# Performance work log

Hardware: AMD Instinct MI355X
Metric: run time of the kernel (lower is better)

## Reference

```python
import jax, jax.numpy as jnp
import numpy as np

H = 8  # num_heads

def layernorm(x, g, b, eps=1e-5):
    mu = jnp.mean(x, axis=-1, keepdims=True)
    var = jnp.var(x, axis=-1, keepdims=True)
    return (x - mu) * jax.lax.rsqrt(var + eps) * g + b

def mha(x, w_in, b_in, w_out, b_out, bias=None):
    # x: [B_, S, D]; w_in: [3D, D] packed q,k,v (PyTorch MHA layout)
    B_, S, D = x.shape
    hd = D // H
    qkv = x @ w_in.T + b_in                      # [B_, S, 3D]
    q, k, v = jnp.split(qkv, 3, axis=-1)
    def heads(t):
        return t.reshape(B_, S, H, hd).transpose(0, 2, 1, 3)  # [B_, H, S, hd]
    q, k, v = heads(q), heads(k), heads(v)
    scores = jnp.einsum('bhqd,bhkd->bhqk', q, k) / jnp.sqrt(jnp.float32(hd))
    if bias is not None:
        scores = scores + bias[None, None]        # broadcast [S,S] bias
    attn = jax.nn.softmax(scores, axis=-1)
    out = jnp.einsum('bhqk,bhkd->bhqd', attn, v)  # [B_, H, S, hd]
    out = out.transpose(0, 2, 1, 3).reshape(B_, S, D)
    return out @ w_out.T + b_out

def setup_inputs() -> dict:
    key = jax.random.key(0)
    ks = jax.random.split(key, 8)
    B, T, N, D, F = 32, 12, 325, 128, 512
    s = 0.05
    return {
        'x': jax.random.normal(ks[0], (B, T, N, D), jnp.float32),
        't_w_in': jax.random.normal(ks[1], (3 * D, D), jnp.float32) * s,
        't_b_in': jnp.zeros((3 * D,), jnp.float32),
        't_w_out': jax.random.normal(ks[2], (D, D), jnp.float32) * s,
        't_b_out': jnp.zeros((D,), jnp.float32),
        's_w_in': jax.random.normal(ks[3], (3 * D, D), jnp.float32) * s,
        's_b_in': jnp.zeros((3 * D,), jnp.float32),
        's_w_out': jax.random.normal(ks[4], (D, D), jnp.float32) * s,
        's_b_out': jnp.zeros((D,), jnp.float32),
        'g_bias': jax.random.normal(ks[5], (N, N), jnp.float32) * 0.5,
        'norm_t_g': jnp.ones((D,), jnp.float32),
        'norm_t_b': jnp.zeros((D,), jnp.float32),
        'norm_s_g': jnp.ones((D,), jnp.float32),
        'norm_s_b': jnp.zeros((D,), jnp.float32),
        'ff_w1': jax.random.normal(ks[6], (F, D), jnp.float32) * s,
        'ff_b1': jnp.zeros((F,), jnp.float32),
        'ff_w2': jax.random.normal(ks[7], (D, F), jnp.float32) * s,
        'ff_b2': jnp.zeros((D,), jnp.float32),
        'norm_ff_g': jnp.ones((D,), jnp.float32),
        'norm_ff_b': jnp.zeros((D,), jnp.float32),
    }

def reference(x, t_w_in, t_b_in, t_w_out, t_b_out, s_w_in, s_b_in, s_w_out, s_b_out,
              g_bias, norm_t_g, norm_t_b, norm_s_g, norm_s_b,
              ff_w1, ff_b1, ff_w2, ff_b2, norm_ff_g, norm_ff_b):
    B, T, N, D = x.shape
    # Temporal attention: each sensor attends over time
    xt = x.transpose(0, 2, 1, 3).reshape(B * N, T, D)
    xt = mha(xt, t_w_in, t_b_in, t_w_out, t_b_out)
    x = layernorm(x + xt.reshape(B, N, T, D).transpose(0, 2, 1, 3), norm_t_g, norm_t_b)
    # Spatial attention with graph bias: each timestep attends over sensors
    xs = x.reshape(B * T, N, D)
    xs = mha(xs, s_w_in, s_b_in, s_w_out, s_b_out, bias=g_bias)
    x = layernorm(x + xs.reshape(B, T, N, D), norm_s_g, norm_s_b)
    # FFN
    h = jax.nn.gelu(x @ ff_w1.T + ff_b1) @ ff_w2.T + ff_b2
    x = layernorm(x + h, norm_ff_g, norm_ff_b)
    return x
```

## Files before the change

kernel.cpp:

```cpp
#include <hip/hip_runtime.h>
#include <cstdint>
#include <cstddef>


#define B_ 32
#define T_ 12
#define N_ 325
#define D_ 128
#define H_ 8
#define F_ 512
#define NT 124800
#define BCH 8
#define CHK (BCH * T_ * N_)
#define NCHUNK 4
#define GT ((CHK + 63) / 64)
#define NKT 11
#define NQT 21

#define O_XBF 0UL
#define O_Y1B 31948800UL
#define O_QKV 63897600UL
#define O_ABUF 87859200UL
#define O_WB 95846400UL
#define O_PB 96370688UL

typedef __attribute__((ext_vector_type(8))) short bf16x8;
typedef __attribute__((ext_vector_type(4))) float f32x4;

__device__ inline float b2f(unsigned short b) {
  unsigned int u = ((unsigned int)b) << 16;
  return __builtin_bit_cast(float, u);
}
__device__ inline unsigned short f2b(float f) {
  unsigned int u = __builtin_bit_cast(unsigned int, f);
  unsigned int r = (u + 0x7FFFu + ((u >> 16) & 1u)) >> 16;
  return (unsigned short)r;
}
__device__ inline f32x4 mfma16(bf16x8 a, bf16x8 b, f32x4 c) {
  return __builtin_amdgcn_mfma_f32_16x16x32_bf16(a, b, c, 0, 0, 0);
}
__device__ inline float gelu_t(float x) {
  float x3 = x * x * x;
  return 0.5f * x * (1.0f + tanhf(0.7978845608f * (x + 0.044715f * x3)));
}

__global__ void k_convert(const void* __restrict__ src, float* __restrict__ dF,
                          unsigned short* __restrict__ dB, long n,
                          const unsigned short* __restrict__ probe) {
  long i = (long)blockIdx.x * blockDim.x + threadIdx.x;
  if (i >= n) return;
  bool isbf = probe[0] != 0;
  float v = isbf ? b2f(((const unsigned short*)src)[i]) : ((const float*)src)[i];
  if (dF) dF[i] = v;
  if (dB) dB[i] = f2b(v);
}

__global__ void k_conv_params(
    const void* s1, const void* s2, const void* s3, const void* s4,
    const void* s5, const void* s6, const void* s7, const void* s8,
    const void* s9, const void* s10, const void* s11, const void* s12,
    const void* s13, const void* s14, const void* s15, const void* s16,
    const void* s17, const void* s18, const void* s19, char* ws,
    const unsigned short* __restrict__ probe) {
  long i = (long)blockIdx.x * blockDim.x + threadIdx.x;
  bool isbf = probe[0] != 0;
  long o = 0;
#define LOADV(src, j) \
  (isbf ? b2f(((const unsigned short*)(src))[j]) : ((const float*)(src))[j])
#define SEGB(src, dstoff, n)                                        \
  if (i < o + (n)) {                                                \
    long j = i - o;                                                 \
    ((unsigned short*)(ws + (dstoff)))[j] = f2b(LOADV(src, j));     \
    return;                                                         \
  }                                                                 \
  o += (n);
#define SEGF(src, dstoff, n)                              \
  if (i < o + (n)) {                                      \
    long j = i - o;                                       \
    ((float*)(ws + (dstoff)))[j] = LOADV(src, j);         \
    return;                                               \
  }                                                       \
  o += (n);
  SEGB(s1, O_WB + 0, 49152)
  SEGF(s2, O_PB + 0, 384)
  SEGB(s3, O_WB + 98304, 16384)
  SEGF(s4, O_PB + 1536, 128)
  SEGB(s5, O_WB + 131072, 49152)
  SEGF(s6, O_PB + 2048, 384)
  SEGB(s7, O_WB + 229376, 16384)
  SEGF(s8, O_PB + 3584, 128)
  SEGF(s9, O_PB + 9728, 105625)
  SEGF(s10, O_PB + 6656, 128)
  SEGF(s11, O_PB + 7168, 128)
  SEGF(s12, O_PB + 7680, 128)
  SEGF(s13, O_PB + 8192, 128)
  SEGB(s14, O_WB + 262144, 65536)
  SEGF(s15, O_PB + 4096, 512)
  SEGB(s16, O_WB + 393216, 65536)
  SEGF(s17, O_PB + 6144, 128)
  SEGF(s18, O_PB + 8704, 128)
  SEGF(s19, O_PB + 9216, 128)
#undef SEGB
#undef SEGF
#undef LOADV
}
#define CONVP_TOTAL 370201L

template <int ROWS, int KTOT>
__device__ inline void stage_tile(short (*dst)[ROWS][32],
                                  const unsigned short* __restrict__ src,
                                  int row0, int k0, int tid, int Mrows) {
  constexpr int CH = ROWS * 16;
#pragma unroll
  for (int it = 0; it < CH / 256; ++it) {
    int cb = tid + it * 256;
    int row = cb >> 4;
    int kc = cb & 15;
    int gr = row0 + row;
    gr = gr < Mrows ? gr : Mrows - 1;
    uint4 v = *(const uint4*)(src + (size_t)gr * KTOT + (size_t)k0 + kc * 8);
    *(uint4*)(&dst[kc >> 2][row][(kc & 3) * 8]) = v;
  }
}

template <int KTOT, bool GELU>
__global__ __launch_bounds__(256) void k_gemm_store(
    const unsigned short* __restrict__ Ab, const unsigned short* __restrict__ Wb,
    const float* __restrict__ bias, unsigned short* __restrict__ outB, int Ntot,
    int Mrows, int Nrows) {
  __shared__ __align__(16) union USm {
    struct { short A[4][64][32]; short B[4][64][32]; } s;
    float C[64][68];
  } sm;
  const int tid = threadIdx.x;
  const int m0 = blockIdx.x * 64;
  const int n0 = blockIdx.y * 64;
  const int lane = tid & 63, wave = tid >> 6;
  const int wm = wave >> 1, wn = wave & 1;
  const int ml = lane & 15, quad = lane >> 4;
  f32x4 acc[2][2] = {};
#pragma unroll
  for (int c = 0; c < KTOT / 128; ++c) {
    if (c) __syncthreads();
    stage_tile<64, KTOT>(sm.s.A, Ab, m0, c * 128, tid, Mrows);
    stage_tile<64, KTOT>(sm.s.B, Wb, n0, c * 128, tid, Nrows);
    __syncthreads();
#pragma unroll
    for (int kc = 0; kc < 4; ++kc) {
      bf16x8 a0 = *(const bf16x8*)&sm.s.A[kc][wm * 32 + ml][quad * 8];
      bf16x8 a1 = *(const bf16x8*)&sm.s.A[kc][wm * 32 + 16 + ml][quad * 8];
      bf16x8 b0 = *(const bf16x8*)&sm.s.B[kc][wn * 32 + ml][quad * 8];
      bf16x8 b1 = *(const bf16x8*)&sm.s.B[kc][wn * 32 + 16 + ml][quad * 8];
      acc[0][0] = mfma16(a0, b0, acc[0][0]);
      acc[0][1] = mfma16(a0, b1, acc[0][1]);
      acc[1][0] = mfma16(a1, b0, acc[1][0]);
      acc[1][1] = mfma16(a1, b1, acc[1][1]);
    }
  }
  __syncthreads();
#pragma unroll
  for (int mi = 0; mi < 2; ++mi)
#pragma unroll
    for (int ni = 0; ni < 2; ++ni)
#pragma unroll
      for (int r = 0; r < 4; ++r)
        sm.C[wm * 32 + mi * 16 + quad * 4 + r][wn * 32 + ni * 16 + ml] =
            acc[mi][ni][r];
  __syncthreads();
  const int trow = tid >> 4;
  const int tcol = (tid & 15) * 4;
  const float4 bv = *(const float4*)&bias[n0 + tcol];
#pragma unroll
  for (int it = 0; it < 4; ++it) {
    int row = it * 16 + trow;
    int gm = m0 + row;
    float4 cv = *(const float4*)&sm.C[row][tcol];
    float v0 = cv.x + bv.x, v1 = cv.y + bv.y, v2 = cv.z + bv.z,
          v3 = cv.w + bv.w;
    if (GELU) {
      v0 = gelu_t(v0); v1 = gelu_t(v1); v2 = gelu_t(v2); v3 = gelu_t(v3);
    }
    if (gm < Mrows) {
      ushort4 ov;
      ov.x = f2b(v0); ov.y = f2b(v1); ov.z = f2b(v2); ov.w = f2b(v3);
      *(ushort4*)&outB[(size_t)gm * Ntot + n0 + tcol] = ov;
    }
  }
}

template <int KTOT, bool FINAL>
__global__ __launch_bounds__(256) void k_gemm_ln(
    const unsigned short* __restrict__ Ab, const unsigned short* __restrict__ Wb,
    const float* __restrict__ bias, const unsigned short* __restrict__ resid,
    const float* __restrict__ gamma, const float* __restrict__ beta,
    unsigned short* __restrict__ outB, void* __restrict__ dOut, size_t row0g,
    const unsigned short* __restrict__ probe, int Mrows) {
  __shared__ __align__(16) union USm {
    struct { short A[4][64][32]; short B[4][128][32]; } s;
    float C[64][132];
  } sm;
  const int tid = threadIdx.x;
  const int m0 = blockIdx.x * 64;
  const int lane = tid & 63, wave = tid >> 6;
  const int wm = wave >> 1, wn = wave & 1;
  const int ml = lane & 15, quad = lane >> 4;
  f32x4 acc[2][4] = {};
#pragma unroll
  for (int c = 0; c < KTOT / 128; ++c) {
    if (c) __syncthreads();
    stage_tile<64, KTOT>(sm.s.A, Ab, m0, c * 128, tid, Mrows);
    stage_tile<128, KTOT>(sm.s.B, Wb, 0, c * 128, tid, 128);
    __syncthreads();
#pragma unroll
    for (int kc = 0; kc < 4; ++kc) {
      bf16x8 a[2], b[4];
#pragma unroll
      for (int mi = 0; mi < 2; ++mi)
        a[mi] = *(const bf16x8*)&sm.s.A[kc][wm * 32 + mi * 16 + ml][quad * 8];
#pragma unroll
      for (int ni = 0; ni < 4; ++ni)
        b[ni] = *(const bf16x8*)&sm.s.B[kc][wn * 64 + ni * 16 + ml][quad * 8];
#pragma unroll
      for (int mi = 0; mi < 2; ++mi)
#pragma unroll
        for (int ni = 0; ni < 4; ++ni)
          acc[mi][ni] = mfma16(a[mi], b[ni], acc[mi][ni]);
    }
  }
  __syncthreads();
#pragma unroll
  for (int mi = 0; mi < 2; ++mi)
#pragma unroll
    for (int ni = 0; ni < 4; ++ni)
#pragma unroll
      for (int r = 0; r < 4; ++r)
        sm.C[wm * 32 + mi * 16 + quad * 4 + r][wn * 64 + ni * 16 + ml] =
            acc[mi][ni][r];
  __syncthreads();
  const int c0 = lane * 2;
  const float bia0 = bias[c0], bia1 = bias[c0 + 1];
  const float ga0 = gamma[c0], ga1 = gamma[c0 + 1];
  const float be0 = beta[c0], be1 = beta[c0 + 1];
  const bool isbf = FINAL ? (probe[0] != 0) : true;
#pragma unroll
  for (int rr = 0; rr < 16; ++rr) {
    int row = wave * 16 + rr;
    int gm = m0 + row;
    bool valid = gm < Mrows;
    float2 cc = *(const float2*)&sm.C[row][c0];
    float r0 = 0.f, r1 = 0.f;
    if (valid) {
      ushort2 rv = *(const ushort2*)&resid[(size_t)gm * 128 + c0];
      r0 = b2f(rv.x);
      r1 = b2f(rv.y);
    }
    float v0 = cc.x + bia0 + r0, v1 = cc.y + bia1 + r1;
    float s = v0 + v1, q = v0 * v0 + v1 * v1;
#pragma unroll
    for (int off = 1; off < 64; off <<= 1) {
      s += __shfl_xor(s, off);
      q += __shfl_xor(q, off);
    }
    float mean = s * (1.f / 128.f);
    float var = q * (1.f / 128.f) - mean * mean;
    float rs = rsqrtf(var + 1e-5f);
    float y0 = (v0 - mean) * rs * ga0 + be0;
    float y1 = (v1 - mean) * rs * ga1 + be1;
    if (valid) {
      if (FINAL) {
        if (isbf) {
          ushort2 ov; ov.x = f2b(y0); ov.y = f2b(y1);
          *(ushort2*)((unsigned short*)dOut + (row0g + gm) * 128 + c0) = ov;
        } else {
          float2 ov; ov.x = y0; ov.y = y1;
          *(float2*)((float*)dOut + (row0g + gm) * 128 + c0) = ov;
        }
      } else {
        ushort2 ov; ov.x = f2b(y0); ov.y = f2b(y1);
        *(ushort2*)&outB[(size_t)gm * 128 + c0] = ov;
      }
    }
  }
}

__global__ __launch_bounds__(128) void k_attn_t(
    const unsigned short* __restrict__ qkv, unsigned short* __restrict__ A) {
  __shared__ float ls[12][384];
  const int tid = threadIdx.x;
  const int bx = blockIdx.x;
  const int b = bx / N_, n = bx % N_;
  for (int i = tid; i < 12 * 384; i += 128) {
    int t = i / 384, c = i % 384;
    size_t tok = (size_t)(b * T_ + t) * N_ + n;
    ls[t][c] = b2f(qkv[tok * 384 + c]);
  }
  __syncthreads();
  if (tid < 96) {
    int h = tid / 12, q = tid % 12;
    const float* qv = &ls[q][h * 16];
    float s[12];
    float m = -1e30f;
#pragma unroll
    for (int t = 0; t < 12; ++t) {
      float d = 0.f;
#pragma unroll
      for (int dd = 0; dd < 16; ++dd) d += qv[dd] * ls[t][128 + h * 16 + dd];
      s[t] = d * 0.25f;
      m = fmaxf(m, s[t]);
    }
    float l = 0.f;
#pragma unroll
    for (int t = 0; t < 12; ++t) {
      s[t] = __expf(s[t] - m);
      l += s[t];
    }
    float inv = 1.0f / l;
    size_t otok = (size_t)(b * T_ + q) * N_ + n;
#pragma unroll
    for (int dd = 0; dd < 16; ++dd) {
      float o = 0.f;
#pragma unroll
      for (int t = 0; t < 12; ++t) o += s[t] * ls[t][256 + h * 16 + dd];
      A[otok * 128 + h * 16 + dd] = f2b(o * inv);
    }
  }
}

__global__ __launch_bounds__(256) void k_attn_s(
    const unsigned short* __restrict__ qkv, const float* __restrict__ gbias,
    unsigned short* __restrict__ A) {
  __shared__ short Ks[352 * 24];
  __shared__ short Vt[16 * 360];
  __shared__ short Ps[4][16 * 40];
  __shared__ uint4 zq;
  const int tid = threadIdx.x;
  const int bt = blockIdx.x, h = blockIdx.y;
  const size_t base = (size_t)bt * N_;
  for (int i = tid; i < 352 * 2; i += 256) {
    int s = i >> 1, half = i & 1;
    if (s < N_) {
      size_t rb = (base + s) * 384 + h * 16 + half * 8;
      uint4 kv = *(const uint4*)(qkv + rb + 128);
      *(uint4*)&Ks[s * 24 + half * 8] = kv;
      uint4 vv = *(const uint4*)(qkv + rb + 256);
      const unsigned short* vs = (const unsigned short*)&vv;
#pragma unroll
      for (int e = 0; e < 8; ++e) Vt[(half * 8 + e) * 360 + s] = vs[e];
    } else {
      *(uint4*)&Ks[s * 24 + half * 8] = uint4{0, 0, 0, 0};
#pragma unroll
      for (int e = 0; e < 8; ++e) Vt[(half * 8 + e) * 360 + s] = 0;
    }
  }
  if (tid == 0) zq = uint4{0, 0, 0, 0};
  __syncthreads();
  const int lane = tid & 63, wave = tid >> 6;
  const int ml = lane & 15, quad = lane >> 4;
  const f32x4 fz = {0.f, 0.f, 0.f, 0.f};
  short* myP = Ps[wave];
  for (int qt = wave; qt < NQT; qt += 4) {
    bf16x8 qfrag = {0, 0, 0, 0, 0, 0, 0, 0};
    int qrow = qt * 16 + ml;
    qrow = qrow < N_ ? qrow : N_ - 1;
    if (quad < 2)
      qfrag = *(const bf16x8*)(qkv + (base + qrow) * 384 + h * 16 + quad * 8);
    f32x4 O = fz;
    float lsum[4] = {0.f, 0.f, 0.f, 0.f};
    for (int kt = 0; kt < NKT; ++kt) {
      const short* kp0 =
          (quad < 2) ? &Ks[(kt * 32 + ml) * 24 + quad * 8] : (const short*)&zq;
      const short* kp1 = (quad < 2) ? &Ks[(kt * 32 + 16 + ml) * 24 + quad * 8]
                                    : (const short*)&zq;
      bf16x8 kf0 = *(const bf16x8*)kp0;
      bf16x8 kf1 = *(const bf16x8*)kp1;
      f32x4 S1 = mfma16(qfrag, kf0, fz);
      f32x4 S2 = mfma16(qfrag, kf1, fz);
      int s0 = kt * 32 + ml, s1g = s0 + 16;
      int sa0 = s0 < N_ ? s0 : N_ - 1;
      int sa1 = s1g < N_ ? s1g : N_ - 1;
      float p1[4], p2[4];
#pragma unroll
      for (int r = 0; r < 4; ++r) {
        int qg = qt * 16 + quad * 4 + r;
        qg = qg < N_ ? qg : N_ - 1;
        const float* brow = gbias + (size_t)qg * N_;
        p1[r] = __expf(S1[r] * 0.25f + brow[sa0]);
        p2[r] = __expf(S2[r] * 0.25f + brow[sa1]);
      }
      if (kt == NKT - 1) {
#pragma unroll
        for (int r = 0; r < 4; ++r) {
          if (s0 >= N_) p1[r] = 0.f;
          if (s1g >= N_) p2[r] = 0.f;
        }
      }
#pragma unroll
      for (int r = 0; r < 4; ++r) {
        lsum[r] += p1[r] + p2[r];
        myP[(quad * 4 + r) * 40 + ml] = (short)f2b(p1[r]);
        myP[(quad * 4 + r) * 40 + 16 + ml] = (short)f2b(p2[r]);
      }
      __builtin_amdgcn_sched_barrier(0);
      bf16x8 pf = *(const bf16x8*)&myP[ml * 40 + quad * 8];
      bf16x8 vf = *(const bf16x8*)&Vt[ml * 360 + kt * 32 + quad * 8];
      O = mfma16(pf, vf, O);
      __builtin_amdgcn_sched_barrier(0);
    }
#pragma unroll
    for (int r = 0; r < 4; ++r) {
      float v = lsum[r];
      v += __shfl_xor(v, 1);
      v += __shfl_xor(v, 2);
      v += __shfl_xor(v, 4);
      v += __shfl_xor(v, 8);
      int qg = qt * 16 + quad * 4 + r;
      if (qg < N_)
        A[(base + qg) * 128 + h * 16 + ml] = f2b(O[r] * (1.f / v));
    }
  }
}

extern "C" void kernel_launch(void* const* d_in, const int* in_sizes, int n_in,
                              void* d_out, int out_size, void* d_ws,
                              size_t ws_size, hipStream_t stream) {
  char* ws = (char*)d_ws;
  const unsigned short* probe = (const unsigned short*)d_in[10];

  unsigned short* xbf = (unsigned short*)(ws + O_XBF);
  unsigned short* y1b = (unsigned short*)(ws + O_Y1B);
  unsigned short* qkvc = (unsigned short*)(ws + O_QKV);
  unsigned short* Abufc = (unsigned short*)(ws + O_ABUF);
  unsigned short* hbuf = qkvc;
  unsigned short* y2b = xbf;
  char* wb = ws + O_WB;
  unsigned short* wt_in = (unsigned short*)(wb + 0);
  unsigned short* wt_out = (unsigned short*)(wb + 98304);
  unsigned short* wsp_in = (unsigned short*)(wb + 131072);
  unsigned short* wsp_out = (unsigned short*)(wb + 229376);
  unsigned short* wff1 = (unsigned short*)(wb + 262144);
  unsigned short* wff2 = (unsigned short*)(wb + 393216);
  char* pb = ws + O_PB;
  float* p_t_b_in = (float*)(pb + 0);
  float* p_t_b_out = (float*)(pb + 1536);
  float* p_s_b_in = (float*)(pb + 2048);
  float* p_s_b_out = (float*)(pb + 3584);
  float* p_ff_b1 = (float*)(pb + 4096);
  float* p_ff_b2 = (float*)(pb + 6144);
  float* p_ntg = (float*)(pb + 6656);
  float* p_ntb = (float*)(pb + 7168);
  float* p_nsg = (float*)(pb + 7680);
  float* p_nsb = (float*)(pb + 8192);
  float* p_nfg = (float*)(pb + 8704);
  float* p_nfb = (float*)(pb + 9216);
  float* p_gbias = (float*)(pb + 9728);

  {
    long n = (long)NT * 128;
    k_convert<<<dim3((unsigned)((n + 255) / 256)), dim3(256), 0, stream>>>(
        d_in[0], nullptr, xbf, n, probe);
    k_conv_params<<<dim3((unsigned)((CONVP_TOTAL + 255) / 256)), dim3(256), 0,
                    stream>>>(d_in[1], d_in[2], d_in[3], d_in[4], d_in[5],
                              d_in[6], d_in[7], d_in[8], d_in[9], d_in[10],
                              d_in[11], d_in[12], d_in[13], d_in[14], d_in[15],
                              d_in[16], d_in[17], d_in[18], d_in[19], ws,
                              probe);
  }

  dim3 blk(256);
  for (int c = 0; c < NCHUNK; ++c) {
    size_t tok0 = (size_t)c * CHK;
    k_gemm_store<128, false><<<dim3(GT, 6), blk, 0, stream>>>(
        xbf + tok0 * 128, wt_in, p_t_b_in, qkvc, 384, CHK, 384);
    k_attn_t<<<dim3(BCH * N_), dim3(128), 0, stream>>>(qkvc, Abufc);
    k_gemm_ln<128, false><<<dim3(GT), blk, 0, stream>>>(
        Abufc, wt_out, p_t_b_out, xbf + tok0 * 128, p_ntg, p_ntb,
        y1b + tok0 * 128, nullptr, 0, probe, CHK);
  }
  for (int c = 0; c < NCHUNK; ++c) {
    size_t tok0 = (size_t)c * CHK;
    k_gemm_store<128, false><<<dim3(GT, 6), blk, 0, stream>>>(
        y1b + tok0 * 128, wsp_in, p_s_b_in, qkvc, 384, CHK, 384);
    k_attn_s<<<dim3(BCH * T_, H_), blk, 0, stream>>>(qkvc, p_gbias, Abufc);
    k_gemm_ln<128, false><<<dim3(GT), blk, 0, stream>>>(
        Abufc, wsp_out, p_s_b_out, y1b + tok0 * 128, p_nsg, p_nsb,
        y2b + tok0 * 128, nullptr, 0, probe, CHK);
  }
  for (int c = 0; c < NCHUNK; ++c) {
    size_t tok0 = (size_t)c * CHK;
    k_gemm_store<128, true><<<dim3(GT, 8), blk, 0, stream>>>(
        y2b + tok0 * 128, wff1, p_ff_b1, hbuf, 512, CHK, 512);
    k_gemm_ln<512, true><<<dim3(GT), blk, 0, stream>>>(
        hbuf, wff2, p_ff_b2, y2b + tok0 * 128, p_nfg, p_nfb, nullptr, d_out,
        tok0, probe, CHK);
  }
}
```

Before: 841.4 us.

## Transpose spatial attention MFMA to keep probabilities in registers, pad bias rows

```diff
diff --git a/kernel.cpp b/kernel.cpp
--- a/kernel.cpp
+++ b/kernel.cpp
@@ -16,6 +16,7 @@
 #define GT ((CHK + 63) / 64)
 #define NKT 11
 #define NQT 21
+#define GBS 328
 
 #define O_XBF 0UL
 #define O_Y1B 31948800UL
@@ -25,6 +26,7 @@
 #define O_PB 96370688UL
 
 typedef __attribute__((ext_vector_type(8))) short bf16x8;
+typedef __attribute__((ext_vector_type(4))) short bf16x4;
 typedef __attribute__((ext_vector_type(4))) float f32x4;
 
 __device__ inline float b2f(unsigned short b) {
@@ -39,6 +41,19 @@
 __device__ inline f32x4 mfma16(bf16x8 a, bf16x8 b, f32x4 c) {
   return __builtin_amdgcn_mfma_f32_16x16x32_bf16(a, b, c, 0, 0, 0);
 }
+#if __has_builtin(__builtin_amdgcn_mfma_f32_16x16x16bf16_1k)
+__device__ inline f32x4 mfma16k16(bf16x4 a, bf16x4 b, f32x4 c) {
+  return __builtin_amdgcn_mfma_f32_16x16x16bf16_1k(a, b, c, 0, 0, 0);
+}
+#else
+__device__ inline f32x4 mfma16k16(bf16x4 a, bf16x4 b, f32x4 c) {
+  f32x4 d;
+  asm volatile("v_mfma_f32_16x16x16_bf16 %0, %1, %2, %3\ns_nop 7\ns_nop 7"
+               : "=v"(d)
+               : "v"(a), "v"(b), "v"(c));
+  return d;
+}
+#endif
 __device__ inline float gelu_t(float x) {
   float x3 = x * x * x;
   return 0.5f * x * (1.0f + tanhf(0.7978845608f * (x + 0.044715f * x3)));
@@ -89,7 +104,14 @@
   SEGF(s6, O_PB + 2048, 384)
   SEGB(s7, O_WB + 229376, 16384)
   SEGF(s8, O_PB + 3584, 128)
-  SEGF(s9, O_PB + 9728, 105625)
+  if (i < o + 105625) {
+    long j = i - o;
+    int q = (int)(j / 325);
+    int s = (int)(j - (long)q * 325);
+    ((float*)(ws + O_PB + 9728))[(size_t)q * GBS + s] = LOADV(s9, j);
+    return;
+  }
+  o += 105625;
   SEGF(s10, O_PB + 6656, 128)
   SEGF(s11, O_PB + 7168, 128)
   SEGF(s12, O_PB + 7680, 128)
@@ -289,10 +311,15 @@
   const int tid = threadIdx.x;
   const int bx = blockIdx.x;
   const int b = bx / N_, n = bx % N_;
-  for (int i = tid; i < 12 * 384; i += 128) {
-    int t = i / 384, c = i % 384;
+  for (int i = tid; i < 576; i += 128) {
+    int t = i / 48, c = (i % 48) * 8;
     size_t tok = (size_t)(b * T_ + t) * N_ + n;
-    ls[t][c] = b2f(qkv[tok * 384 + c]);
+    uint4 v = *(const uint4*)(qkv + tok * 384 + c);
+    const unsigned short* pv = (const unsigned short*)&v;
+    float4 f0 = {b2f(pv[0]), b2f(pv[1]), b2f(pv[2]), b2f(pv[3])};
+    float4 f1 = {b2f(pv[4]), b2f(pv[5]), b2f(pv[6]), b2f(pv[7])};
+    *(float4*)&ls[t][c] = f0;
+    *(float4*)&ls[t][c + 4] = f1;
   }
   __syncthreads();
   if (tid < 96) {
@@ -315,23 +342,30 @@
       l += s[t];
     }
     float inv = 1.0f / l;
+    float o[16];
+#pragma unroll
+    for (int dd = 0; dd < 16; ++dd) {
+      float acc = 0.f;
+#pragma unroll
+      for (int t = 0; t < 12; ++t) acc += s[t] * ls[t][256 + h * 16 + dd];
+      o[dd] = acc * inv;
+    }
     size_t otok = (size_t)(b * T_ + q) * N_ + n;
 #pragma unroll
-    for (int dd = 0; dd < 16; ++dd) {
-      float o = 0.f;
-#pragma unroll
-      for (int t = 0; t < 12; ++t) o += s[t] * ls[t][256 + h * 16 + dd];
-      A[otok * 128 + h * 16 + dd] = f2b(o * inv);
+    for (int g = 0; g < 4; ++g) {
+      ushort4 ov;
+      ov.x = f2b(o[g * 4 + 0]); ov.y = f2b(o[g * 4 + 1]);
+      ov.z = f2b(o[g * 4 + 2]); ov.w = f2b(o[g * 4 + 3]);
+      *(ushort4*)&A[otok * 128 + h * 16 + g * 4] = ov;
     }
   }
 }
 
 __global__ __launch_bounds__(256) void k_attn_s(
-    const unsigned short* __restrict__ qkv, const float* __restrict__ gbias,
+    const unsigned short* __restrict__ qkv, const float* __restrict__ gbp,
     unsigned short* __restrict__ A) {
   __shared__ short Ks[352 * 24];
-  __shared__ short Vt[16 * 360];
-  __shared__ short Ps[4][16 * 40];
+  __shared__ short Vt[16 * 364];
   __shared__ uint4 zq;
   const int tid = threadIdx.x;
   const int bt = blockIdx.x, h = blockIdx.y;
@@ -345,11 +379,11 @@
       uint4 vv = *(const uint4*)(qkv + rb + 256);
       const unsigned short* vs = (const unsigned short*)&vv;
 #pragma unroll
-      for (int e = 0; e < 8; ++e) Vt[(half * 8 + e) * 360 + s] = vs[e];
+      for (int e = 0; e < 8; ++e) Vt[(half * 8 + e) * 364 + s] = vs[e];
     } else {
       *(uint4*)&Ks[s * 24 + half * 8] = uint4{0, 0, 0, 0};
 #pragma unroll
-      for (int e = 0; e < 8; ++e) Vt[(half * 8 + e) * 360 + s] = 0;
+      for (int e = 0; e < 8; ++e) Vt[(half * 8 + e) * 364 + s] = 0;
     }
   }
   if (tid == 0) zq = uint4{0, 0, 0, 0};
@@ -357,65 +391,62 @@
   const int lane = tid & 63, wave = tid >> 6;
   const int ml = lane & 15, quad = lane >> 4;
   const f32x4 fz = {0.f, 0.f, 0.f, 0.f};
-  short* myP = Ps[wave];
   for (int qt = wave; qt < NQT; qt += 4) {
+    int q = qt * 16 + ml;
+    int qc = q < N_ ? q : N_ - 1;
     bf16x8 qfrag = {0, 0, 0, 0, 0, 0, 0, 0};
-    int qrow = qt * 16 + ml;
-    qrow = qrow < N_ ? qrow : N_ - 1;
     if (quad < 2)
-      qfrag = *(const bf16x8*)(qkv + (base + qrow) * 384 + h * 16 + quad * 8);
+      qfrag = *(const bf16x8*)(qkv + (base + qc) * 384 + h * 16 + quad * 8);
+    const float* gb = gbp + (size_t)qc * GBS;
     f32x4 O = fz;
-    float lsum[4] = {0.f, 0.f, 0.f, 0.f};
+    float lsum = 0.f;
     for (int kt = 0; kt < NKT; ++kt) {
+      const int sb = kt * 32;
       const short* kp0 =
-          (quad < 2) ? &Ks[(kt * 32 + ml) * 24 + quad * 8] : (const short*)&zq;
-      const short* kp1 = (quad < 2) ? &Ks[(kt * 32 + 16 + ml) * 24 + quad * 8]
-                                    : (const short*)&zq;
+          (quad < 2) ? &Ks[(sb + ml) * 24 + quad * 8] : (const short*)&zq;
+      const short* kp1 =
+          (quad < 2) ? &Ks[(sb + 16 + ml) * 24 + quad * 8] : (const short*)&zq;
       bf16x8 kf0 = *(const bf16x8*)kp0;
       bf16x8 kf1 = *(const bf16x8*)kp1;
-      f32x4 S1 = mfma16(qfrag, kf0, fz);
-      f32x4 S2 = mfma16(qfrag, kf1, fz);
-      int s0 = kt * 32 + ml, s1g = s0 + 16;
-      int sa0 = s0 < N_ ? s0 : N_ - 1;
-      int sa1 = s1g < N_ ? s1g : N_ - 1;
-      float p1[4], p2[4];
-#pragma unroll
-      for (int r = 0; r < 4; ++r) {
-        int qg = qt * 16 + quad * 4 + r;
-        qg = qg < N_ ? qg : N_ - 1;
-        const float* brow = gbias + (size_t)qg * N_;
-        p1[r] = __expf(S1[r] * 0.25f + brow[sa0]);
-        p2[r] = __expf(S2[r] * 0.25f + brow[sa1]);
-      }
+      f32x4 S0 = mfma16(kf0, qfrag, fz);
+      f32x4 S1 = mfma16(kf1, qfrag, fz);
+      float4 g0 = *(const float4*)&gb[sb + quad * 4];
+      const int sb1 = (sb + 16 <= 292) ? sb + 16 : 292;
+      float4 g1 = *(const float4*)&gb[sb1 + quad * 4];
+      float p0[4], p1[4];
+      p0[0] = __expf(S0[0] * 0.25f + g0.x);
+      p0[1] = __expf(S0[1] * 0.25f + g0.y);
+      p0[2] = __expf(S0[2] * 0.25f + g0.z);
+      p0[3] = __expf(S0[3] * 0.25f + g0.w);
+      p1[0] = __expf(S1[0] * 0.25f + g1.x);
+      p1[1] = __expf(S1[1] * 0.25f + g1.y);
+      p1[2] = __expf(S1[2] * 0.25f + g1.z);
+      p1[3] = __expf(S1[3] * 0.25f + g1.w);
       if (kt == NKT - 1) {
 #pragma unroll
         for (int r = 0; r < 4; ++r) {
-          if (s0 >= N_) p1[r] = 0.f;
-          if (s1g >= N_) p2[r] = 0.f;
+          if (sb + quad * 4 + r >= N_) p0[r] = 0.f;
+          p1[r] = 0.f;
         }
       }
-#pragma unroll
-      for (int r = 0; r < 4; ++r) {
-        lsum[r] += p1[r] + p2[r];
-        myP[(quad * 4 + r) * 40 + ml] = (short)f2b(p1[r]);
-        myP[(quad * 4 + r) * 40 + 16 + ml] = (short)f2b(p2[r]);
-      }
-      __builtin_amdgcn_sched_barrier(0);
-      bf16x8 pf = *(const bf16x8*)&myP[ml * 40 + quad * 8];
-      bf16x8 vf = *(const bf16x8*)&Vt[ml * 360 + kt * 32 + quad * 8];
-      O = mfma16(pf, vf, O);
-      __builtin_amdgcn_sched_barrier(0);
-    }
+      lsum += p0[0] + p0[1] + p0[2] + p0[3] + p1[0] + p1[1] + p1[2] + p1[3];
+      bf16x4 a0 = {(short)f2b(p0[0]), (short)f2b(p0[1]), (short)f2b(p0[2]),
+                   (short)f2b(p0[3])};
+      bf16x4 a1 = {(short)f2b(p1[0]), (short)f2b(p1[1]), (short)f2b(p1[2]),
+                   (short)f2b(p1[3])};
+      bf16x4 v0 = *(const bf16x4*)&Vt[ml * 364 + sb + quad * 4];
+      bf16x4 v1 = *(const bf16x4*)&Vt[ml * 364 + sb + 16 + quad * 4];
+      O = mfma16k16(a0, v0, O);
+      O = mfma16k16(a1, v1, O);
+    }
+    lsum += __shfl_xor(lsum, 16);
+    lsum += __shfl_xor(lsum, 32);
 #pragma unroll
     for (int r = 0; r < 4; ++r) {
-      float v = lsum[r];
-      v += __shfl_xor(v, 1);
-      v += __shfl_xor(v, 2);
-      v += __shfl_xor(v, 4);
-      v += __shfl_xor(v, 8);
       int qg = qt * 16 + quad * 4 + r;
+      float sr = __shfl(lsum, quad * 4 + r);
       if (qg < N_)
-        A[(base + qg) * 128 + h * 16 + ml] = f2b(O[r] * (1.f / v));
+        A[(base + qg) * 128 + h * 16 + ml] = f2b(O[r] * (1.f / sr));
     }
   }
 }
@@ -452,7 +483,7 @@
   float* p_nsb = (float*)(pb + 8192);
   float* p_nfg = (float*)(pb + 8704);
   float* p_nfb = (float*)(pb + 9216);
-  float* p_gbias = (float*)(pb + 9728);
+  float* p_gbp = (float*)(pb + 9728);
 
   {
     long n = (long)NT * 128;
@@ -480,7 +511,7 @@
     size_t tok0 = (size_t)c * CHK;
     k_gemm_store<128, false><<<dim3(GT, 6), blk, 0, stream>>>(
         y1b + tok0 * 128, wsp_in, p_s_b_in, qkvc, 384, CHK, 384);
-    k_attn_s<<<dim3(BCH * T_, H_), blk, 0, stream>>>(qkvc, p_gbias, Abufc);
+    k_attn_s<<<dim3(BCH * T_, H_), blk, 0, stream>>>(qkvc, p_gbp, Abufc);
     k_gemm_ln<128, false><<<dim3(GT), blk, 0, stream>>>(
         Abufc, wsp_out, p_s_b_out, y1b + tok0 * 128, p_nsg, p_nsb,
         y2b + tok0 * 128, nullptr, 0, probe, CHK);
```

Result: faster. 766.3 us (-8.9%).
